# Kernel tuning notes

Hardware: AMD Instinct MI355X
Metric: run time of the kernel (lower is better)

The kernel has to match this reference:

```python
import jax, jax.numpy as jnp
import numpy as np

B = 4096
ED = 128          # EMBEDDING_DIM
HD = 64           # HIDDEN_DIM
LH = 128          # LSTM_HIDDEN_DIM
IN_DIM = ED * (12 + 48 + 1)  # 7808
N_ABILITY, N_MOVE = 300, 900


def setup_inputs() -> dict:
    key = jax.random.key(0)
    ks = jax.random.split(key, 16)
    s = lambda k, shape, scale=0.05: (jax.random.normal(k, shape, dtype=jnp.float32) * scale)
    return {
        "ability_ids": jax.random.randint(ks[0], (B, 12), 0, N_ABILITY),
        "move_ids": jax.random.randint(ks[1], (B, 48), 0, N_MOVE),
        "numerical": s(ks[2], (B, 84), 1.0),
        "mask": (jax.random.uniform(ks[3], (B, 9)) > 0.3).astype(jnp.float32),
        "h0": jnp.zeros((B, LH), jnp.float32),
        "c0": jnp.zeros((B, LH), jnp.float32),
        "ability_emb": s(ks[4], (N_ABILITY, ED), 1.0),
        "move_emb": s(ks[5], (N_MOVE, ED), 1.0),
        "num_W": s(ks[6], (ED, 84)),
        "num_b": s(ks[7], (ED,)),
        "Wih": s(ks[8], (4 * LH, IN_DIM), 0.01),
        "Whh": s(ks[9], (4 * LH, LH)),
        "bih": s(ks[10], (4 * LH,)),
        "bhh": s(ks[11], (4 * LH,)),
        "W1": s(ks[12], (HD, LH)),
        "b1": s(ks[13], (HD,)),
        "W2": s(ks[14], (ED, HD)),
        "b2": s(ks[15], (ED,)),
        "Wa": s(jax.random.fold_in(key, 100), (9, ED)),
        "ba": s(jax.random.fold_in(key, 101), (9,)),
    }


def reference(ability_ids, move_ids, numerical, mask, h0, c0,
              ability_emb, move_emb, num_W, num_b,
              Wih, Whh, bih, bhh, W1, b1, W2, b2, Wa, ba):
    # Gather + concat: [B, 12*ED] + [B, 48*ED] + [B, ED] -> [B, 7808]
    ab = ability_emb[ability_ids].reshape(ability_ids.shape[0], 12 * ED)
    mv = move_emb[move_ids].reshape(move_ids.shape[0], 48 * ED)
    num = numerical @ num_W.T + num_b
    x = jnp.concatenate([ab, mv, num], axis=-1)

    # Single-timestep LSTM (torch gate order: i, f, g, o)
    gates = x @ Wih.T + bih + h0 @ Whh.T + bhh
    i, f, g, o = jnp.split(gates, 4, axis=-1)
    i, f, o = jax.nn.sigmoid(i), jax.nn.sigmoid(f), jax.nn.sigmoid(o)
    g = jnp.tanh(g)
    c1 = f * c0 + i * g
    h1 = o * jnp.tanh(c1)

    # MLP head + action logits
    feat = jax.nn.relu(h1 @ W1.T + b1) @ W2.T + b2
    probs = jax.nn.softmax(feat @ Wa.T + ba, axis=-1)

    # Masked renormalization; fall back to unmasked probs when mask kills everything
    masked = probs * mask
    ssum = masked.sum(-1, keepdims=True)
    out = jnp.where(ssum > 0, masked / jnp.where(ssum > 0, ssum, 1.0), probs)
    return out, h1, c1
```

## Files before the change

### kernel.cpp

```cpp
#include <hip/hip_runtime.h>
#include <hip/hip_bf16.h>
#include <stdint.h>
#include <stddef.h>

typedef __bf16 bf16;
typedef __bf16 bf16x4 __attribute__((ext_vector_type(4)));
typedef __bf16 bf16x8 __attribute__((ext_vector_type(8)));
typedef float f32x4 __attribute__((ext_vector_type(4)));

#define BATCH 4096
#define KIH 7808
#define KTOT 7936
#define NG 512
#define LH 128
#define HD 64
#define ED 128
#define SPLITK 4

#define OFF_WCAT 0u
#define OFF_GPART 8126464u
#define OFF_XT   24903680u
#define OFF_AB   27000832u
#define OFF_MV   27077632u
#define OFF_ADDR 27308032u
#define OFF_H1B  28356608u
#define OFF_W1F  29405184u
#define OFF_W2F  29421568u
#define OFF_WAF  29437952u
#define OFF_NB   29442048u

#define O_H1 (BATCH * 9)
#define O_C1 (BATCH * 9 + BATCH * LH)

#define PREP_BP 2048
#define PREP_CW (PREP_BP + 512)
#define PREP_CE (PREP_CW + 150)
#define PREP_TOT (PREP_CE + 1)

typedef const __attribute__((address_space(1))) uint32_t* gas_ptr;
typedef __attribute__((address_space(3))) uint32_t* las_ptr;

__device__ __forceinline__ void async16(const void* g, void* l) {
    __builtin_amdgcn_global_load_lds((gas_ptr)g, (las_ptr)l, 16, 0, 0);
}

__global__ void prep(const int* __restrict__ ab_ids,
                     const int* __restrict__ mv_ids,
                     const float* __restrict__ numerical,
                     const float* __restrict__ h0,
                     const float* __restrict__ numW,
                     const float* __restrict__ numb,
                     const float* __restrict__ Wih,
                     const float* __restrict__ Whh,
                     const float* __restrict__ ab_emb,
                     const float* __restrict__ mv_emb,
                     const float* __restrict__ W1,
                     const float* __restrict__ W2,
                     const float* __restrict__ Wa,
                     uint8_t* __restrict__ ws) {
    const int bid = blockIdx.x;
    const int t = threadIdx.x;

    if (bid < PREP_BP) {
        bf16* xtail = (bf16*)(ws + OFF_XT);
        uint32_t* addrs = (uint32_t*)(ws + OFF_ADDR);
        const int h = t >> 7;
        const int th = t & 127;
        const int b = bid * 2 + h;

        __shared__ int ids[2][60];
        if (th < 60)
            ids[h][th] = (th < 12) ? ab_ids[b * 12 + th]
                                   : mv_ids[b * 48 + (th - 12)];

        const float v = (th < 84) ? numerical[(size_t)b * 84 + th] : 0.f;
        xtail[(size_t)b * 256 + th] = (bf16)v;
        xtail[(size_t)b * 256 + 128 + th] = (bf16)h0[(size_t)b * LH + th];
        __syncthreads();

        if (th < 64) {
            uint32_t off;
            if (th < 12) off = OFF_AB + (uint32_t)ids[h][th] * 256u;
            else if (th < 60) off = OFF_MV + (uint32_t)ids[h][th] * 256u;
            else if (th == 60) off = OFF_XT + (uint32_t)b * 512u;
            else if (th == 61) off = OFF_XT + (uint32_t)b * 512u + 256u;
            else off = OFF_XT;
            addrs[(size_t)b * 64 + th] = off;
        }
    } else if (bid < PREP_CW) {
        bf16* Wcat = (bf16*)(ws + OFF_WCAT);
        float* nbias = (float*)(ws + OFF_NB);
        const int n = bid - PREP_BP;

        __shared__ float wrow[128];
        __shared__ float nbs[128];
        if (t < 128) wrow[t] = Wih[(size_t)n * KIH + 7680 + t];
        else nbs[t - 128] = numb[t - 128];
        __syncthreads();

        const float* src_ih = Wih + (size_t)n * KIH;
        bf16* dst = Wcat + (size_t)n * KTOT;
        for (int k4 = t; k4 < 1920; k4 += 256) {
            const int k = k4 * 4;
            const float4 v = *(const float4*)(src_ih + k);
            bf16x4 o = {(bf16)v.x, (bf16)v.y, (bf16)v.z, (bf16)v.w};
            *(bf16x4*)(dst + k) = o;
        }
        if (t < 84) {
            float acc = 0.f;
#pragma unroll 4
            for (int e = 0; e < 128; ++e)
                acc += wrow[e] * numW[e * 84 + t];
            dst[7680 + t] = (bf16)acc;
        } else if (t < 128) {
            dst[7680 + t] = (bf16)0.f;
        } else {
            const int tt = t - 128;
            dst[KIH + tt] = (bf16)Whh[(size_t)n * LH + tt];
        }
        if (t == 255) {
            float a = 0.f;
#pragma unroll 4
            for (int e = 0; e < 128; ++e) a += wrow[e] * nbs[e];
            nbias[n] = a;
        }
    } else if (bid < PREP_CE) {
        bf16* ab8 = (bf16*)(ws + OFF_AB);
        bf16* mv8 = (bf16*)(ws + OFF_MV);
        const int i = ((bid - PREP_CW) * 256 + t) * 4;
        const bool isab = i < 300 * 128;
        const float4 v = isab ? *(const float4*)(ab_emb + i)
                              : *(const float4*)(mv_emb + (i - 300 * 128));
        bf16x4 o = {(bf16)v.x, (bf16)v.y, (bf16)v.z, (bf16)v.w};
        if (isab) *(bf16x4*)(ab8 + i) = o;
        else *(bf16x4*)(mv8 + (i - 300 * 128)) = o;
    } else {
        bf16* W1f = (bf16*)(ws + OFF_W1F);
        bf16* W2f = (bf16*)(ws + OFF_W2F);
        bf16* Waf = (bf16*)(ws + OFF_WAF);
        for (int e = t; e < 8192; e += 256) {
            const int j = e & 7, ln = (e >> 3) & 63, fid = e >> 9;
            const int kt = fid & 3, nt = fid >> 2;
            const int n = nt * 16 + (ln & 15);
            const int k = kt * 32 + (ln >> 4) * 8 + j;
            W1f[e] = (bf16)W1[n * 128 + k];
        }
        for (int e = t; e < 8192; e += 256) {
            const int j = e & 7, ln = (e >> 3) & 63, fid = e >> 9;
            const int kt = fid & 1, nt = fid >> 1;
            const int n = nt * 16 + (ln & 15);
            const int k = kt * 32 + (ln >> 4) * 8 + j;
            W2f[e] = (bf16)W2[n * 64 + k];
        }
        for (int e = t; e < 2048; e += 256) {
            const int j = e & 7, ln = (e >> 3) & 63, kt = e >> 9;
            const int n = ln & 15;
            const int k = kt * 32 + (ln >> 4) * 8 + j;
            Waf[e] = (n < 9) ? (bf16)Wa[n * 128 + k] : (bf16)0.f;
        }
    }
}

__global__ __launch_bounds__(256, 2) void gemm_gates(
    const uint8_t* __restrict__ wsbase,
    const bf16* __restrict__ Wcat,
    const uint32_t* __restrict__ addrs,
    bf16* __restrict__ gpart) {
    __shared__ bf16 As[2][128 * 64];
    __shared__ bf16 Bs[2][128 * 64];
    __shared__ uint32_t adr[17][128];

    const int tid = threadIdx.x;
    const int w = tid >> 6;
    const int lane = tid & 63;
    const int bm = blockIdx.x;
    const int bn = blockIdx.y;
    const int bz = blockIdx.z;
    const int kt_beg = bz * 31;
    const int kt_end = kt_beg + 31;

    const int s0 = kt_beg >> 1;
    const int ns = ((kt_end - 1) >> 1) - s0 + 1;
    for (int i = tid; i < ns * 128; i += 256) {
        adr[i >> 7][i & 127] =
            addrs[(size_t)(bm * 128 + (i & 127)) * 64 + s0 + (i >> 7)];
    }

    const int r_l = lane >> 3;
    const int sc16 = ((lane & 7) ^ r_l) * 16;

    const int wn = w & 1;
    const int wk = w >> 1;
    const int n0 = wn * 64;
    const int kk8 = wk * 4 + (lane >> 4);
    const int fl = lane & 15;

    f32x4 acc[8][4];
#pragma unroll
    for (int i = 0; i < 8; ++i)
#pragma unroll
        for (int j = 0; j < 4; ++j)
#pragma unroll
            for (int r = 0; r < 4; ++r) acc[i][j][r] = 0.f;

    __syncthreads();

    auto stage = [&](int kt, int pb) {
        const int k0 = kt * 64;
        const int sl = (kt >> 1) - s0;
        const int hb = (kt & 1) * 128;
#pragma unroll
        for (int j = 0; j < 4; ++j) {
            const int row = (w * 4 + j) * 8 + r_l;
            const uint8_t* gsrc = wsbase + adr[sl][row] + hb + sc16;
            async16(gsrc, (void*)&As[pb][((w * 4 + j) * 64 + lane) * 8]);
        }
#pragma unroll
        for (int j = 0; j < 4; ++j) {
            const int row = (w * 4 + j) * 8 + r_l;
            const bf16* gsrc = Wcat + (size_t)(bn * 128 + row) * KTOT + k0 + (sc16 >> 1);
            async16(gsrc, (void*)&Bs[pb][((w * 4 + j) * 64 + lane) * 8]);
        }
    };

    stage(kt_beg, 0);

    for (int kt = kt_beg; kt < kt_end; ++kt) {
        const int pb = (kt - kt_beg) & 1;
        __syncthreads();
        if (kt + 1 < kt_end) stage(kt + 1, pb ^ 1);

        const bf16* Ab = &As[pb][0];
        const bf16* Bb = &Bs[pb][0];

        bf16x8 bfr[4];
#pragma unroll
        for (int tj = 0; tj < 4; ++tj) {
            const int n = n0 + tj * 16 + fl;
            bfr[tj] = *(const bf16x8*)&Bb[n * 64 + ((kk8 ^ (n & 7)) * 8)];
        }
#pragma unroll
        for (int ti = 0; ti < 8; ++ti) {
            const int m = ti * 16 + fl;
            const bf16x8 af = *(const bf16x8*)&Ab[m * 64 + ((kk8 ^ (m & 7)) * 8)];
#pragma unroll
            for (int tj = 0; tj < 4; ++tj)
                acc[ti][tj] = __builtin_amdgcn_mfma_f32_16x16x32_bf16(
                    af, bfr[tj], acc[ti][tj], 0, 0, 0);
        }
    }

    __syncthreads();
    float* red = (wn == 0) ? (float*)&As[0][0] : (float*)&Bs[0][0];
    if (wk == 1) {
#pragma unroll
        for (int ti = 0; ti < 8; ++ti)
#pragma unroll
            for (int tj = 0; tj < 4; ++tj)
#pragma unroll
                for (int r = 0; r < 4; ++r)
                    red[((ti * 4 + tj) * 4 + r) * 64 + lane] = acc[ti][tj][r];
    }
    __syncthreads();

    if (wk == 0) {
        bf16* gdst = gpart + (size_t)bz * BATCH * NG;
        const int mlo = (lane >> 4) * 4;
#pragma unroll
        for (int ti = 0; ti < 8; ++ti)
#pragma unroll
            for (int tj = 0; tj < 4; ++tj) {
                const int mg = bm * 128 + ti * 16 + mlo;
                const int ng = bn * 128 + n0 + tj * 16 + fl;
                bf16* dst = gdst + (size_t)mg * NG + ng;
#pragma unroll
                for (int r = 0; r < 4; ++r)
                    dst[(size_t)r * NG] = (bf16)(
                        acc[ti][tj][r] + red[((ti * 4 + tj) * 4 + r) * 64 + lane]);
            }
    }
}

__global__ void reduce_lstm(const bf16* __restrict__ gpart,
                            const float* __restrict__ bih,
                            const float* __restrict__ bhh,
                            const float* __restrict__ nbias,
                            const float* __restrict__ c0,
                            float* __restrict__ out,
                            bf16* __restrict__ h1b) {
    const int t = threadIdx.x;
    const int b = blockIdx.x * 2 + (t >> 7);
    const int u = t & 127;

    float gv[4];
#pragma unroll
    for (int q = 0; q < 4; ++q)
        gv[q] = bih[q * 128 + u] + bhh[q * 128 + u] + nbias[q * 128 + u];
#pragma unroll
    for (int z = 0; z < SPLITK; ++z) {
        const bf16* gz = gpart + ((size_t)z * BATCH + b) * NG + u;
#pragma unroll
        for (int q = 0; q < 4; ++q) gv[q] += (float)gz[q * 128];
    }

    const float iv = 1.f / (1.f + __expf(-gv[0]));
    const float fv = 1.f / (1.f + __expf(-gv[1]));
    const float gg = tanhf(gv[2]);
    const float ov = 1.f / (1.f + __expf(-gv[3]));
    const float c1 = fv * c0[(size_t)b * LH + u] + iv * gg;
    const float h1 = ov * tanhf(c1);

    out[O_H1 + (size_t)b * LH + u] = h1;
    out[O_C1 + (size_t)b * LH + u] = c1;
    h1b[(size_t)b * LH + u] = (bf16)h1;
}

__global__ __launch_bounds__(64) void mlp_head(
    const bf16* __restrict__ h1b, const float* __restrict__ mask,
    const bf16* __restrict__ W1f, const bf16* __restrict__ W2f,
    const bf16* __restrict__ Waf,
    const float* __restrict__ b1, const float* __restrict__ b2,
    const float* __restrict__ ba,
    float* __restrict__ out) {
    __shared__ bf16 uS[16 * 64];
    __shared__ bf16 fS[16 * 128];

    const int lane = threadIdx.x;
    const int b0 = blockIdx.x * 16;
    const int nl = lane & 15, kg = lane >> 4;

    bf16x8 ah[4];
#pragma unroll
    for (int kt = 0; kt < 4; ++kt)
        ah[kt] = *(const bf16x8*)&h1b[(size_t)(b0 + nl) * 128 + kt * 32 + kg * 8];

#pragma unroll
    for (int nt = 0; nt < 4; ++nt) {
        f32x4 a = {0.f, 0.f, 0.f, 0.f};
#pragma unroll
        for (int kt = 0; kt < 4; ++kt)
            a = __builtin_amdgcn_mfma_f32_16x16x32_bf16(
                ah[kt], *(const bf16x8*)&W1f[((nt * 4 + kt) * 64 + lane) * 8],
                a, 0, 0, 0);
        const int n = nt * 16 + nl;
        const float bb = b1[n];
#pragma unroll
        for (int r = 0; r < 4; ++r)
            uS[(kg * 4 + r) * 64 + n] = (bf16)fmaxf(a[r] + bb, 0.f);
    }
    __syncthreads();

    bf16x8 au[2];
#pragma unroll
    for (int kt = 0; kt < 2; ++kt)
        au[kt] = *(const bf16x8*)&uS[nl * 64 + kt * 32 + kg * 8];

#pragma unroll
    for (int nt = 0; nt < 8; ++nt) {
        f32x4 a = {0.f, 0.f, 0.f, 0.f};
#pragma unroll
        for (int kt = 0; kt < 2; ++kt)
            a = __builtin_amdgcn_mfma_f32_16x16x32_bf16(
                au[kt], *(const bf16x8*)&W2f[((nt * 2 + kt) * 64 + lane) * 8],
                a, 0, 0, 0);
        const int n = nt * 16 + nl;
        const float bb = b2[n];
#pragma unroll
        for (int r = 0; r < 4; ++r)
            fS[(kg * 4 + r) * 128 + n] = (bf16)(a[r] + bb);
    }
    __syncthreads();

    bf16x8 afr[4];
#pragma unroll
    for (int kt = 0; kt < 4; ++kt)
        afr[kt] = *(const bf16x8*)&fS[nl * 128 + kt * 32 + kg * 8];

    f32x4 lg4 = {0.f, 0.f, 0.f, 0.f};
#pragma unroll
    for (int kt = 0; kt < 4; ++kt)
        lg4 = __builtin_amdgcn_mfma_f32_16x16x32_bf16(
            afr[kt], *(const bf16x8*)&Waf[(kt * 64 + lane) * 8], lg4, 0, 0, 0);

    const float bav = (nl < 9) ? ba[nl] : 0.f;

#pragma unroll
    for (int r = 0; r < 4; ++r) {
        const int b = b0 + kg * 4 + r;
        float lg = (nl < 9) ? lg4[r] + bav : -1e30f;
        float mx = lg;
#pragma unroll
        for (int off = 1; off < 16; off <<= 1)
            mx = fmaxf(mx, __shfl_xor(mx, off, 64));
        const float e = (nl < 9) ? __expf(lg - mx) : 0.f;
        const float mv = (nl < 9) ? mask[(size_t)b * 9 + nl] : 0.f;
        float tot = e, ms = e * mv;
#pragma unroll
        for (int off = 1; off < 16; off <<= 1) {
            tot += __shfl_xor(tot, off, 64);
            ms += __shfl_xor(ms, off, 64);
        }
        if (nl < 9)
            out[(size_t)b * 9 + nl] = (ms > 0.f) ? e * mv / ms : e / tot;
    }
}

extern "C" void kernel_launch(void* const* d_in, const int* in_sizes, int n_in,
                              void* d_out, int out_size, void* d_ws, size_t ws_size,
                              hipStream_t stream) {
    const int* ab_ids = (const int*)d_in[0];
    const int* mv_ids = (const int*)d_in[1];
    const float* numerical = (const float*)d_in[2];
    const float* mask = (const float*)d_in[3];
    const float* h0 = (const float*)d_in[4];
    const float* c0 = (const float*)d_in[5];
    const float* ab_emb = (const float*)d_in[6];
    const float* mv_emb = (const float*)d_in[7];
    const float* numW = (const float*)d_in[8];
    const float* numb = (const float*)d_in[9];
    const float* Wih = (const float*)d_in[10];
    const float* Whh = (const float*)d_in[11];
    const float* bih = (const float*)d_in[12];
    const float* bhh = (const float*)d_in[13];
    const float* W1 = (const float*)d_in[14];
    const float* b1 = (const float*)d_in[15];
    const float* W2 = (const float*)d_in[16];
    const float* b2 = (const float*)d_in[17];
    const float* Wa = (const float*)d_in[18];
    const float* ba = (const float*)d_in[19];
    float* out = (float*)d_out;

    uint8_t* ws = (uint8_t*)d_ws;
    bf16* Wcat = (bf16*)(ws + OFF_WCAT);
    bf16* gpart = (bf16*)(ws + OFF_GPART);
    uint32_t* addrs = (uint32_t*)(ws + OFF_ADDR);
    bf16* h1b = (bf16*)(ws + OFF_H1B);
    bf16* W1f = (bf16*)(ws + OFF_W1F);
    bf16* W2f = (bf16*)(ws + OFF_W2F);
    bf16* Waf = (bf16*)(ws + OFF_WAF);
    float* nbias = (float*)(ws + OFF_NB);

    prep<<<PREP_TOT, 256, 0, stream>>>(
        ab_ids, mv_ids, numerical, h0, numW, numb, Wih, Whh, ab_emb, mv_emb,
        W1, W2, Wa, ws);
    gemm_gates<<<dim3(32, 4, SPLITK), 256, 0, stream>>>(ws, Wcat, addrs, gpart);
    reduce_lstm<<<BATCH / 2, 256, 0, stream>>>(gpart, bih, bhh, nbias, c0,
                                               out, h1b);
    mlp_head<<<BATCH / 16, 64, 0, stream>>>(h1b, mask, W1f, W2f, Waf,
                                            b1, b2, ba, out);
}
```

Baseline: 169.0 us.

## Fuse four kernels into one cooperative persistent kernel with grid syncs

Replaces the prep, split-K gate GEMM, LSTM reduce and MLP head launches with a single cooperative kernel of 512 blocks that uses grid.sync between phases. The LSTM reduction and MLP head are also merged, so h1 stays in shared memory instead of being written out and read back. The aim is to remove launch gaps and one global round-trip. The cost is that all blocks must be co-resident (launch bounds of 2 blocks per CU), plus grid-wide barrier overhead and idle blocks in the tail phase. It falls back to the old multi-kernel path if the cooperative launch fails.

Result: slower. 420.3 us (+148.7%).

```diff
diff --git a/kernel.cpp b/kernel.cpp
--- a/kernel.cpp
+++ b/kernel.cpp
@@ -1,4 +1,5 @@
 #include <hip/hip_runtime.h>
+#include <hip/hip_cooperative_groups.h>
 #include <hip/hip_bf16.h>
 #include <stdint.h>
 #include <stddef.h>
@@ -16,6 +17,7 @@
 #define HD 64
 #define ED 128
 #define SPLITK 4
+#define GRID 512
 
 #define OFF_WCAT 0u
 #define OFF_GPART 8126464u
@@ -402,6 +404,396 @@
         }
         if (nl < 9)
             out[(size_t)b * 9 + nl] = (ms > 0.f) ? e * mv / ms : e / tot;
+    }
+}
+
+__global__ __launch_bounds__(256, 2) void fused(
+    const int* __restrict__ ab_ids, const int* __restrict__ mv_ids,
+    const float* __restrict__ numerical, const float* __restrict__ mask,
+    const float* __restrict__ h0, const float* __restrict__ c0,
+    const float* __restrict__ ab_emb, const float* __restrict__ mv_emb,
+    const float* __restrict__ numW, const float* __restrict__ numb,
+    const float* __restrict__ Wih, const float* __restrict__ Whh,
+    const float* __restrict__ bih, const float* __restrict__ bhh,
+    const float* __restrict__ W1, const float* __restrict__ b1,
+    const float* __restrict__ W2, const float* __restrict__ b2,
+    const float* __restrict__ Wa, const float* __restrict__ ba,
+    uint8_t* __restrict__ ws, float* __restrict__ out) {
+
+    __shared__ bf16 As[2][128 * 64];
+    __shared__ bf16 Bs[2][128 * 64];
+    __shared__ uint32_t adr[17][128];
+
+    const int bid = blockIdx.x;
+    const int t = threadIdx.x;
+    cooperative_groups::grid_group grid = cooperative_groups::this_grid();
+
+    for (int vb = bid; vb < PREP_TOT; vb += GRID) {
+        if (vb < PREP_BP) {
+            bf16* xtail = (bf16*)(ws + OFF_XT);
+            uint32_t* addrs = (uint32_t*)(ws + OFF_ADDR);
+            int* ids = (int*)&adr[0][0];
+            const int h = t >> 7;
+            const int th = t & 127;
+            const int b = vb * 2 + h;
+
+            if (th < 60)
+                ids[h * 60 + th] = (th < 12) ? ab_ids[b * 12 + th]
+                                             : mv_ids[b * 48 + (th - 12)];
+
+            const float v = (th < 84) ? numerical[(size_t)b * 84 + th] : 0.f;
+            xtail[(size_t)b * 256 + th] = (bf16)v;
+            xtail[(size_t)b * 256 + 128 + th] = (bf16)h0[(size_t)b * LH + th];
+            __syncthreads();
+
+            if (th < 64) {
+                uint32_t off;
+                if (th < 12) off = OFF_AB + (uint32_t)ids[h * 60 + th] * 256u;
+                else if (th < 60) off = OFF_MV + (uint32_t)ids[h * 60 + th] * 256u;
+                else if (th == 60) off = OFF_XT + (uint32_t)b * 512u;
+                else if (th == 61) off = OFF_XT + (uint32_t)b * 512u + 256u;
+                else off = OFF_XT;
+                addrs[(size_t)b * 64 + th] = off;
+            }
+        } else if (vb < PREP_CW) {
+            bf16* Wcat = (bf16*)(ws + OFF_WCAT);
+            float* nbias = (float*)(ws + OFF_NB);
+            const int n = vb - PREP_BP;
+            float* wrow = (float*)&As[0][0];
+            float* nbs = wrow + 128;
+
+            if (t < 128) wrow[t] = Wih[(size_t)n * KIH + 7680 + t];
+            else if (t < 256) nbs[t - 128] = numb[t - 128];
+            __syncthreads();
+
+            const float* src_ih = Wih + (size_t)n * KIH;
+            bf16* dst = Wcat + (size_t)n * KTOT;
+            for (int k4 = t; k4 < 1920; k4 += 256) {
+                const int k = k4 * 4;
+                const float4 v = *(const float4*)(src_ih + k);
+                bf16x4 o = {(bf16)v.x, (bf16)v.y, (bf16)v.z, (bf16)v.w};
+                *(bf16x4*)(dst + k) = o;
+            }
+            if (t < 84) {
+                float acc = 0.f;
+#pragma unroll 4
+                for (int e = 0; e < 128; ++e)
+                    acc += wrow[e] * numW[e * 84 + t];
+                dst[7680 + t] = (bf16)acc;
+            } else if (t < 128) {
+                dst[7680 + t] = (bf16)0.f;
+            } else {
+                const int tt = t - 128;
+                dst[KIH + tt] = (bf16)Whh[(size_t)n * LH + tt];
+            }
+            if (t == 255) {
+                float a = 0.f;
+#pragma unroll 4
+                for (int e = 0; e < 128; ++e) a += wrow[e] * nbs[e];
+                nbias[n] = a;
+            }
+        } else if (vb < PREP_CE) {
+            bf16* ab8 = (bf16*)(ws + OFF_AB);
+            bf16* mv8 = (bf16*)(ws + OFF_MV);
+            const int i = ((vb - PREP_CW) * 256 + t) * 4;
+            const bool isab = i < 300 * 128;
+            const float4 v = isab ? *(const float4*)(ab_emb + i)
+                                  : *(const float4*)(mv_emb + (i - 300 * 128));
+            bf16x4 o = {(bf16)v.x, (bf16)v.y, (bf16)v.z, (bf16)v.w};
+            if (isab) *(bf16x4*)(ab8 + i) = o;
+            else *(bf16x4*)(mv8 + (i - 300 * 128)) = o;
+        } else {
+            bf16* W1f = (bf16*)(ws + OFF_W1F);
+            bf16* W2f = (bf16*)(ws + OFF_W2F);
+            bf16* Waf = (bf16*)(ws + OFF_WAF);
+            for (int e = t; e < 8192; e += 256) {
+                const int j = e & 7, ln = (e >> 3) & 63, fid = e >> 9;
+                const int kt = fid & 3, nt = fid >> 2;
+                const int n = nt * 16 + (ln & 15);
+                const int k = kt * 32 + (ln >> 4) * 8 + j;
+                W1f[e] = (bf16)W1[n * 128 + k];
+            }
+            for (int e = t; e < 8192; e += 256) {
+                const int j = e & 7, ln = (e >> 3) & 63, fid = e >> 9;
+                const int kt = fid & 1, nt = fid >> 1;
+                const int n = nt * 16 + (ln & 15);
+                const int k = kt * 32 + (ln >> 4) * 8 + j;
+                W2f[e] = (bf16)W2[n * 64 + k];
+            }
+            for (int e = t; e < 2048; e += 256) {
+                const int j = e & 7, ln = (e >> 3) & 63, kt = e >> 9;
+                const int n = ln & 15;
+                const int k = kt * 32 + (ln >> 4) * 8 + j;
+                Waf[e] = (n < 9) ? (bf16)Wa[n * 128 + k] : (bf16)0.f;
+            }
+        }
+        __syncthreads();
+    }
+
+    __threadfence();
+    grid.sync();
+
+    {
+        const uint8_t* wsbase = ws;
+        const bf16* Wcat = (const bf16*)(ws + OFF_WCAT);
+        const uint32_t* addrs = (const uint32_t*)(ws + OFF_ADDR);
+        bf16* gpart = (bf16*)(ws + OFF_GPART);
+
+        const int w = t >> 6;
+        const int lane = t & 63;
+        const int bm = bid & 31;
+        const int bn = (bid >> 5) & 3;
+        const int bz = bid >> 7;
+        const int kt_beg = bz * 31;
+        const int kt_end = kt_beg + 31;
+
+        const int s0 = kt_beg >> 1;
+        const int ns = ((kt_end - 1) >> 1) - s0 + 1;
+        for (int i = t; i < ns * 128; i += 256) {
+            adr[i >> 7][i & 127] =
+                addrs[(size_t)(bm * 128 + (i & 127)) * 64 + s0 + (i >> 7)];
+        }
+
+        const int r_l = lane >> 3;
+        const int sc16 = ((lane & 7) ^ r_l) * 16;
+
+        const int wn = w & 1;
+        const int wk = w >> 1;
+        const int n0 = wn * 64;
+        const int kk8 = wk * 4 + (lane >> 4);
+        const int fl = lane & 15;
+
+        f32x4 acc[8][4];
+#pragma unroll
+        for (int i = 0; i < 8; ++i)
+#pragma unroll
+            for (int j = 0; j < 4; ++j)
+#pragma unroll
+                for (int r = 0; r < 4; ++r) acc[i][j][r] = 0.f;
+
+        __syncthreads();
+
+        auto stage = [&](int kt, int pb) {
+            const int k0 = kt * 64;
+            const int sl = (kt >> 1) - s0;
+            const int hb = (kt & 1) * 128;
+#pragma unroll
+            for (int j = 0; j < 4; ++j) {
+                const int row = (w * 4 + j) * 8 + r_l;
+                const uint8_t* gsrc = wsbase + adr[sl][row] + hb + sc16;
+                async16(gsrc, (void*)&As[pb][((w * 4 + j) * 64 + lane) * 8]);
+            }
+#pragma unroll
+            for (int j = 0; j < 4; ++j) {
+                const int row = (w * 4 + j) * 8 + r_l;
+                const bf16* gsrc = Wcat + (size_t)(bn * 128 + row) * KTOT + k0 + (sc16 >> 1);
+                async16(gsrc, (void*)&Bs[pb][((w * 4 + j) * 64 + lane) * 8]);
+            }
+        };
+
+        stage(kt_beg, 0);
+
+        for (int kt = kt_beg; kt < kt_end; ++kt) {
+            const int pb = (kt - kt_beg) & 1;
+            __syncthreads();
+            if (kt + 1 < kt_end) stage(kt + 1, pb ^ 1);
+
+            const bf16* Ab = &As[pb][0];
+            const bf16* Bb = &Bs[pb][0];
+
+            bf16x8 bfr[4];
+#pragma unroll
+            for (int tj = 0; tj < 4; ++tj) {
+                const int n = n0 + tj * 16 + fl;
+                bfr[tj] = *(const bf16x8*)&Bb[n * 64 + ((kk8 ^ (n & 7)) * 8)];
+            }
+#pragma unroll
+            for (int ti = 0; ti < 8; ++ti) {
+                const int m = ti * 16 + fl;
+                const bf16x8 af = *(const bf16x8*)&Ab[m * 64 + ((kk8 ^ (m & 7)) * 8)];
+#pragma unroll
+                for (int tj = 0; tj < 4; ++tj)
+                    acc[ti][tj] = __builtin_amdgcn_mfma_f32_16x16x32_bf16(
+                        af, bfr[tj], acc[ti][tj], 0, 0, 0);
+            }
+        }
+
+        __syncthreads();
+        float* red = (wn == 0) ? (float*)&As[0][0] : (float*)&Bs[0][0];
+        if (wk == 1) {
+#pragma unroll
+            for (int ti = 0; ti < 8; ++ti)
+#pragma unroll
+                for (int tj = 0; tj < 4; ++tj)
+#pragma unroll
+                    for (int r = 0; r < 4; ++r)
+                        red[((ti * 4 + tj) * 4 + r) * 64 + lane] = acc[ti][tj][r];
+        }
+        __syncthreads();
+
+        if (wk == 0) {
+            bf16* gdst = gpart + (size_t)bz * BATCH * NG;
+            const int mlo = (lane >> 4) * 4;
+#pragma unroll
+            for (int ti = 0; ti < 8; ++ti)
+#pragma unroll
+                for (int tj = 0; tj < 4; ++tj) {
+                    const int mg = bm * 128 + ti * 16 + mlo;
+                    const int ng = bn * 128 + n0 + tj * 16 + fl;
+                    bf16* dst = gdst + (size_t)mg * NG + ng;
+#pragma unroll
+                    for (int r = 0; r < 4; ++r)
+                        dst[(size_t)r * NG] = (bf16)(
+                            acc[ti][tj][r] + red[((ti * 4 + tj) * 4 + r) * 64 + lane]);
+                }
+        }
+    }
+
+    __threadfence();
+    grid.sync();
+
+    if (bid < 256) {
+        const bf16* gpart = (const bf16*)(ws + OFF_GPART);
+        const float* nbias = (const float*)(ws + OFF_NB);
+        bf16* hS = (bf16*)&As[0][0];
+        bf16* uS = (bf16*)&Bs[0][0];
+        bf16* fS = uS + 16 * 64;
+
+        {
+            const int r = t >> 4;
+            const int uc = (t & 15) * 8;
+            const int b = bid * 16 + r;
+
+            float gv[4][8];
+#pragma unroll
+            for (int q = 0; q < 4; ++q)
+#pragma unroll
+                for (int hh = 0; hh < 2; ++hh) {
+                    const f32x4 va = *(const f32x4*)(bih + q * 128 + uc + hh * 4);
+                    const f32x4 vb = *(const f32x4*)(bhh + q * 128 + uc + hh * 4);
+                    const f32x4 vn = *(const f32x4*)(nbias + q * 128 + uc + hh * 4);
+#pragma unroll
+                    for (int j = 0; j < 4; ++j)
+                        gv[q][hh * 4 + j] = va[j] + vb[j] + vn[j];
+                }
+#pragma unroll
+            for (int z = 0; z < SPLITK; ++z) {
+                const bf16* gz = gpart + ((size_t)z * BATCH + b) * NG;
+#pragma unroll
+                for (int q = 0; q < 4; ++q) {
+                    const bf16x8 v = *(const bf16x8*)(gz + q * 128 + uc);
+#pragma unroll
+                    for (int j = 0; j < 8; ++j) gv[q][j] += (float)v[j];
+                }
+            }
+
+            const f32x4 c0a = *(const f32x4*)(c0 + (size_t)b * LH + uc);
+            const f32x4 c0b = *(const f32x4*)(c0 + (size_t)b * LH + uc + 4);
+            float h1v[8], c1v[8];
+#pragma unroll
+            for (int j = 0; j < 8; ++j) {
+                const float iv = 1.f / (1.f + __expf(-gv[0][j]));
+                const float fv = 1.f / (1.f + __expf(-gv[1][j]));
+                const float gg = tanhf(gv[2][j]);
+                const float ov = 1.f / (1.f + __expf(-gv[3][j]));
+                const float c0j = (j < 4) ? c0a[j] : c0b[j - 4];
+                const float c1 = fv * c0j + iv * gg;
+                const float h1 = ov * tanhf(c1);
+                c1v[j] = c1;
+                h1v[j] = h1;
+                hS[r * 128 + uc + j] = (bf16)h1;
+            }
+            *(f32x4*)(out + O_H1 + (size_t)b * LH + uc) = *(const f32x4*)&h1v[0];
+            *(f32x4*)(out + O_H1 + (size_t)b * LH + uc + 4) = *(const f32x4*)&h1v[4];
+            *(f32x4*)(out + O_C1 + (size_t)b * LH + uc) = *(const f32x4*)&c1v[0];
+            *(f32x4*)(out + O_C1 + (size_t)b * LH + uc + 4) = *(const f32x4*)&c1v[4];
+        }
+        __syncthreads();
+
+        const bf16* W1f = (const bf16*)(ws + OFF_W1F);
+        const bf16* W2f = (const bf16*)(ws + OFF_W2F);
+        const bf16* Waf = (const bf16*)(ws + OFF_WAF);
+        const int nl = t & 15, kg = (t & 63) >> 4;
+        const int b0 = bid * 16;
+
+        if (t < 64) {
+            bf16x8 ah[4];
+#pragma unroll
+            for (int kt = 0; kt < 4; ++kt)
+                ah[kt] = *(const bf16x8*)&hS[nl * 128 + kt * 32 + kg * 8];
+#pragma unroll
+            for (int nt = 0; nt < 4; ++nt) {
+                f32x4 a = {0.f, 0.f, 0.f, 0.f};
+#pragma unroll
+                for (int kt = 0; kt < 4; ++kt)
+                    a = __builtin_amdgcn_mfma_f32_16x16x32_bf16(
+                        ah[kt], *(const bf16x8*)&W1f[((nt * 4 + kt) * 64 + t) * 8],
+                        a, 0, 0, 0);
+                const int n = nt * 16 + nl;
+                const float bb = b1[n];
+#pragma unroll
+                for (int rr = 0; rr < 4; ++rr)
+                    uS[(kg * 4 + rr) * 64 + n] = (bf16)fmaxf(a[rr] + bb, 0.f);
+            }
+        }
+        __syncthreads();
+
+        if (t < 64) {
+            bf16x8 au[2];
+#pragma unroll
+            for (int kt = 0; kt < 2; ++kt)
+                au[kt] = *(const bf16x8*)&uS[nl * 64 + kt * 32 + kg * 8];
+#pragma unroll
+            for (int nt = 0; nt < 8; ++nt) {
+                f32x4 a = {0.f, 0.f, 0.f, 0.f};
+#pragma unroll
+                for (int kt = 0; kt < 2; ++kt)
+                    a = __builtin_amdgcn_mfma_f32_16x16x32_bf16(
+                        au[kt], *(const bf16x8*)&W2f[((nt * 2 + kt) * 64 + t) * 8],
+                        a, 0, 0, 0);
+                const int n = nt * 16 + nl;
+                const float bb = b2[n];
+#pragma unroll
+                for (int rr = 0; rr < 4; ++rr)
+                    fS[(kg * 4 + rr) * 128 + n] = (bf16)(a[rr] + bb);
+            }
+        }
+        __syncthreads();
+
+        if (t < 64) {
+            bf16x8 afr[4];
+#pragma unroll
+            for (int kt = 0; kt < 4; ++kt)
+                afr[kt] = *(const bf16x8*)&fS[nl * 128 + kt * 32 + kg * 8];
+
+            f32x4 lg4 = {0.f, 0.f, 0.f, 0.f};
+#pragma unroll
+            for (int kt = 0; kt < 4; ++kt)
+                lg4 = __builtin_amdgcn_mfma_f32_16x16x32_bf16(
+                    afr[kt], *(const bf16x8*)&Waf[(kt * 64 + t) * 8], lg4, 0, 0, 0);
+
+            const float bav = (nl < 9) ? ba[nl] : 0.f;
+
+#pragma unroll
+            for (int rr = 0; rr < 4; ++rr) {
+                const int b = b0 + kg * 4 + rr;
+                float lg = (nl < 9) ? lg4[rr] + bav : -1e30f;
+                float mx = lg;
+#pragma unroll
+                for (int off = 1; off < 16; off <<= 1)
+                    mx = fmaxf(mx, __shfl_xor(mx, off, 64));
+                const float e = (nl < 9) ? __expf(lg - mx) : 0.f;
+                const float mv = (nl < 9) ? mask[(size_t)b * 9 + nl] : 0.f;
+                float tot = e, ms = e * mv;
+#pragma unroll
+                for (int off = 1; off < 16; off <<= 1) {
+                    tot += __shfl_xor(tot, off, 64);
+                    ms += __shfl_xor(ms, off, 64);
+                }
+                if (nl < 9)
+                    out[(size_t)b * 9 + nl] = (ms > 0.f) ? e * mv / ms : e / tot;
+            }
+        }
     }
 }
 
@@ -429,23 +821,48 @@
     const float* Wa = (const float*)d_in[18];
     const float* ba = (const float*)d_in[19];
     float* out = (float*)d_out;
-
     uint8_t* ws = (uint8_t*)d_ws;
-    bf16* Wcat = (bf16*)(ws + OFF_WCAT);
-    bf16* gpart = (bf16*)(ws + OFF_GPART);
-    uint32_t* addrs = (uint32_t*)(ws + OFF_ADDR);
-    bf16* h1b = (bf16*)(ws + OFF_H1B);
-    bf16* W1f = (bf16*)(ws + OFF_W1F);
-    bf16* W2f = (bf16*)(ws + OFF_W2F);
-    bf16* Waf = (bf16*)(ws + OFF_WAF);
-    float* nbias = (float*)(ws + OFF_NB);
-
-    prep<<<PREP_TOT, 256, 0, stream>>>(
-        ab_ids, mv_ids, numerical, h0, numW, numb, Wih, Whh, ab_emb, mv_emb,
-        W1, W2, Wa, ws);
-    gemm_gates<<<dim3(32, 4, SPLITK), 256, 0, stream>>>(ws, Wcat, addrs, gpart);
-    reduce_lstm<<<BATCH / 2, 256, 0, stream>>>(gpart, bih, bhh, nbias, c0,
-                                               out, h1b);
-    mlp_head<<<BATCH / 16, 64, 0, stream>>>(h1b, mask, W1f, W2f, Waf,
-                                            b1, b2, ba, out);
+
+    static int s_coop = -1;
+    if (s_coop < 0) {
+        int dev = 0;
+        hipGetDevice(&dev);
+        int v = 0;
+        hipDeviceGetAttribute(&v, hipDeviceAttributeCooperativeLaunch, dev);
+        s_coop = v;
+    }
+
+    bool launched = false;
+    if (s_coop) {
+        void* args[22] = {
+            (void*)&ab_ids, (void*)&mv_ids, (void*)&numerical, (void*)&mask,
+            (void*)&h0, (void*)&c0, (void*)&ab_emb, (void*)&mv_emb,
+            (void*)&numW, (void*)&numb, (void*)&Wih, (void*)&Whh,
+            (void*)&bih, (void*)&bhh, (void*)&W1, (void*)&b1,
+            (void*)&W2, (void*)&b2, (void*)&Wa, (void*)&ba,
+            (void*)&ws, (void*)&out};
+        launched = (hipLaunchCooperativeKernel((const void*)fused, dim3(GRID),
+                                               dim3(256), args, 0, stream) ==
+                    hipSuccess);
+    }
+
+    if (!launched) {
+        bf16* Wcat = (bf16*)(ws + OFF_WCAT);
+        bf16* gpart = (bf16*)(ws + OFF_GPART);
+        uint32_t* addrs = (uint32_t*)(ws + OFF_ADDR);
+        bf16* h1b = (bf16*)(ws + OFF_H1B);
+        bf16* W1f = (bf16*)(ws + OFF_W1F);
+        bf16* W2f = (bf16*)(ws + OFF_W2F);
+        bf16* Waf = (bf16*)(ws + OFF_WAF);
+        float* nbias = (float*)(ws + OFF_NB);
+
+        prep<<<PREP_TOT, 256, 0, stream>>>(
+            ab_ids, mv_ids, numerical, h0, numW, numb, Wih, Whh, ab_emb, mv_emb,
+            W1, W2, Wa, ws);
+        gemm_gates<<<dim3(32, 4, SPLITK), 256, 0, stream>>>(ws, Wcat, addrs, gpart);
+        reduce_lstm<<<BATCH / 2, 256, 0, stream>>>(gpart, bih, bhh, nbias, c0,
+                                                   out, h1b);
+        mlp_head<<<BATCH / 16, 64, 0, stream>>>(h1b, mask, W1f, W2f, Waf,
+                                                b1, b2, ba, out);
+    }
 }
```

## Fuse LSTM reduction with MLP head and remap GEMM blocks per XCD

Applied to the files above, without the earlier changes.

The split-K reduction plus LSTM cell and the MLP/softmax head are merged into one tail kernel. h1 now stays in shared memory as bf16 instead of going through a global workspace buffer, which removes one launch and a global round-trip. The reduction loads are vectorised, each thread handling 8 units. Separately, the GEMM grid is flattened to 1D and block ids are remapped so that blocks landing on the same XCD share a bn column, for better L2 reuse of weight tiles. The cost is that only one of the four waves in each tail block does the MLP work, leaving the rest idle during that phase.

Result: no change. 168.4 us (-0.3%).

```diff
diff --git a/kernel.cpp b/kernel.cpp
--- a/kernel.cpp
+++ b/kernel.cpp
@@ -23,7 +23,6 @@
 #define OFF_AB   27000832u
 #define OFF_MV   27077632u
 #define OFF_ADDR 27308032u
-#define OFF_H1B  28356608u
 #define OFF_W1F  29405184u
 #define OFF_W2F  29421568u
 #define OFF_WAF  29437952u
@@ -173,9 +172,15 @@
     const int tid = threadIdx.x;
     const int w = tid >> 6;
     const int lane = tid & 63;
-    const int bm = blockIdx.x;
-    const int bn = blockIdx.y;
-    const int bz = blockIdx.z;
+
+    const int bid = blockIdx.x;
+    const int xcd = bid & 7;
+    const int slot = bid >> 3;
+    const int bn = xcd & 3;
+    const int combo = ((xcd >> 2) << 6) + slot;
+    const int bm = combo & 31;
+    const int bz = combo >> 5;
+
     const int kt_beg = bz * 31;
     const int kt_end = kt_beg + 31;
 
@@ -281,127 +286,156 @@
     }
 }
 
-__global__ void reduce_lstm(const bf16* __restrict__ gpart,
-                            const float* __restrict__ bih,
-                            const float* __restrict__ bhh,
-                            const float* __restrict__ nbias,
-                            const float* __restrict__ c0,
-                            float* __restrict__ out,
-                            bf16* __restrict__ h1b) {
-    const int t = threadIdx.x;
-    const int b = blockIdx.x * 2 + (t >> 7);
-    const int u = t & 127;
-
-    float gv[4];
-#pragma unroll
-    for (int q = 0; q < 4; ++q)
-        gv[q] = bih[q * 128 + u] + bhh[q * 128 + u] + nbias[q * 128 + u];
-#pragma unroll
-    for (int z = 0; z < SPLITK; ++z) {
-        const bf16* gz = gpart + ((size_t)z * BATCH + b) * NG + u;
-#pragma unroll
-        for (int q = 0; q < 4; ++q) gv[q] += (float)gz[q * 128];
-    }
-
-    const float iv = 1.f / (1.f + __expf(-gv[0]));
-    const float fv = 1.f / (1.f + __expf(-gv[1]));
-    const float gg = tanhf(gv[2]);
-    const float ov = 1.f / (1.f + __expf(-gv[3]));
-    const float c1 = fv * c0[(size_t)b * LH + u] + iv * gg;
-    const float h1 = ov * tanhf(c1);
-
-    out[O_H1 + (size_t)b * LH + u] = h1;
-    out[O_C1 + (size_t)b * LH + u] = c1;
-    h1b[(size_t)b * LH + u] = (bf16)h1;
-}
-
-__global__ __launch_bounds__(64) void mlp_head(
-    const bf16* __restrict__ h1b, const float* __restrict__ mask,
+__global__ __launch_bounds__(256) void tail(
+    const bf16* __restrict__ gpart,
+    const float* __restrict__ bih, const float* __restrict__ bhh,
+    const float* __restrict__ nbias, const float* __restrict__ c0,
+    const float* __restrict__ mask,
     const bf16* __restrict__ W1f, const bf16* __restrict__ W2f,
     const bf16* __restrict__ Waf,
     const float* __restrict__ b1, const float* __restrict__ b2,
     const float* __restrict__ ba,
     float* __restrict__ out) {
+    __shared__ bf16 hS[16 * 128];
     __shared__ bf16 uS[16 * 64];
     __shared__ bf16 fS[16 * 128];
 
-    const int lane = threadIdx.x;
-    const int b0 = blockIdx.x * 16;
-    const int nl = lane & 15, kg = lane >> 4;
-
-    bf16x8 ah[4];
-#pragma unroll
-    for (int kt = 0; kt < 4; ++kt)
-        ah[kt] = *(const bf16x8*)&h1b[(size_t)(b0 + nl) * 128 + kt * 32 + kg * 8];
-
-#pragma unroll
-    for (int nt = 0; nt < 4; ++nt) {
-        f32x4 a = {0.f, 0.f, 0.f, 0.f};
+    const int t = threadIdx.x;
+    const int bid = blockIdx.x;
+    const int b0 = bid * 16;
+
+    {
+        const int r = t >> 4;
+        const int uc = (t & 15) * 8;
+        const int b = b0 + r;
+
+        float gv[4][8];
+#pragma unroll
+        for (int q = 0; q < 4; ++q)
+#pragma unroll
+            for (int hh = 0; hh < 2; ++hh) {
+                const f32x4 va = *(const f32x4*)(bih + q * 128 + uc + hh * 4);
+                const f32x4 vb = *(const f32x4*)(bhh + q * 128 + uc + hh * 4);
+                const f32x4 vn = *(const f32x4*)(nbias + q * 128 + uc + hh * 4);
+#pragma unroll
+                for (int j = 0; j < 4; ++j)
+                    gv[q][hh * 4 + j] = va[j] + vb[j] + vn[j];
+            }
+#pragma unroll
+        for (int z = 0; z < SPLITK; ++z) {
+            const bf16* gz = gpart + ((size_t)z * BATCH + b) * NG;
+#pragma unroll
+            for (int q = 0; q < 4; ++q) {
+                const bf16x8 v = *(const bf16x8*)(gz + q * 128 + uc);
+#pragma unroll
+                for (int j = 0; j < 8; ++j) gv[q][j] += (float)v[j];
+            }
+        }
+
+        const f32x4 c0a = *(const f32x4*)(c0 + (size_t)b * LH + uc);
+        const f32x4 c0b = *(const f32x4*)(c0 + (size_t)b * LH + uc + 4);
+        float h1v[8], c1v[8];
+        bf16x8 hv8;
+#pragma unroll
+        for (int j = 0; j < 8; ++j) {
+            const float iv = 1.f / (1.f + __expf(-gv[0][j]));
+            const float fv = 1.f / (1.f + __expf(-gv[1][j]));
+            const float gg = tanhf(gv[2][j]);
+            const float ov = 1.f / (1.f + __expf(-gv[3][j]));
+            const float c0j = (j < 4) ? c0a[j] : c0b[j - 4];
+            const float c1 = fv * c0j + iv * gg;
+            const float h1 = ov * tanhf(c1);
+            c1v[j] = c1;
+            h1v[j] = h1;
+            hv8[j] = (bf16)h1;
+        }
+        *(bf16x8*)&hS[r * 128 + uc] = hv8;
+        *(f32x4*)(out + O_H1 + (size_t)b * LH + uc) = *(const f32x4*)&h1v[0];
+        *(f32x4*)(out + O_H1 + (size_t)b * LH + uc + 4) = *(const f32x4*)&h1v[4];
+        *(f32x4*)(out + O_C1 + (size_t)b * LH + uc) = *(const f32x4*)&c1v[0];
+        *(f32x4*)(out + O_C1 + (size_t)b * LH + uc + 4) = *(const f32x4*)&c1v[4];
+    }
+    __syncthreads();
+
+    const int nl = t & 15, kg = (t & 63) >> 4;
+
+    if (t < 64) {
+        bf16x8 ah[4];
 #pragma unroll
         for (int kt = 0; kt < 4; ++kt)
-            a = __builtin_amdgcn_mfma_f32_16x16x32_bf16(
-                ah[kt], *(const bf16x8*)&W1f[((nt * 4 + kt) * 64 + lane) * 8],
-                a, 0, 0, 0);
-        const int n = nt * 16 + nl;
-        const float bb = b1[n];
-#pragma unroll
-        for (int r = 0; r < 4; ++r)
-            uS[(kg * 4 + r) * 64 + n] = (bf16)fmaxf(a[r] + bb, 0.f);
-    }
-    __syncthreads();
-
-    bf16x8 au[2];
-#pragma unroll
-    for (int kt = 0; kt < 2; ++kt)
-        au[kt] = *(const bf16x8*)&uS[nl * 64 + kt * 32 + kg * 8];
-
-#pragma unroll
-    for (int nt = 0; nt < 8; ++nt) {
-        f32x4 a = {0.f, 0.f, 0.f, 0.f};
+            ah[kt] = *(const bf16x8*)&hS[nl * 128 + kt * 32 + kg * 8];
+#pragma unroll
+        for (int nt = 0; nt < 4; ++nt) {
+            f32x4 a = {0.f, 0.f, 0.f, 0.f};
+#pragma unroll
+            for (int kt = 0; kt < 4; ++kt)
+                a = __builtin_amdgcn_mfma_f32_16x16x32_bf16(
+                    ah[kt], *(const bf16x8*)&W1f[((nt * 4 + kt) * 64 + t) * 8],
+                    a, 0, 0, 0);
+            const int n = nt * 16 + nl;
+            const float bb = b1[n];
+#pragma unroll
+            for (int rr = 0; rr < 4; ++rr)
+                uS[(kg * 4 + rr) * 64 + n] = (bf16)fmaxf(a[rr] + bb, 0.f);
+        }
+    }
+    __syncthreads();
+
+    if (t < 64) {
+        bf16x8 au[2];
 #pragma unroll
         for (int kt = 0; kt < 2; ++kt)
-            a = __builtin_amdgcn_mfma_f32_16x16x32_bf16(
-                au[kt], *(const bf16x8*)&W2f[((nt * 2 + kt) * 64 + lane) * 8],
-                a, 0, 0, 0);
-        const int n = nt * 16 + nl;
-        const float bb = b2[n];
-#pragma unroll
-        for (int r = 0; r < 4; ++r)
-            fS[(kg * 4 + r) * 128 + n] = (bf16)(a[r] + bb);
-    }
-    __syncthreads();
-
-    bf16x8 afr[4];
-#pragma unroll
-    for (int kt = 0; kt < 4; ++kt)
-        afr[kt] = *(const bf16x8*)&fS[nl * 128 + kt * 32 + kg * 8];
-
-    f32x4 lg4 = {0.f, 0.f, 0.f, 0.f};
-#pragma unroll
-    for (int kt = 0; kt < 4; ++kt)
-        lg4 = __builtin_amdgcn_mfma_f32_16x16x32_bf16(
-            afr[kt], *(const bf16x8*)&Waf[(kt * 64 + lane) * 8], lg4, 0, 0, 0);
-
-    const float bav = (nl < 9) ? ba[nl] : 0.f;
-
-#pragma unroll
-    for (int r = 0; r < 4; ++r) {
-        const int b = b0 + kg * 4 + r;
-        float lg = (nl < 9) ? lg4[r] + bav : -1e30f;
-        float mx = lg;
-#pragma unroll
-        for (int off = 1; off < 16; off <<= 1)
-            mx = fmaxf(mx, __shfl_xor(mx, off, 64));
-        const float e = (nl < 9) ? __expf(lg - mx) : 0.f;
-        const float mv = (nl < 9) ? mask[(size_t)b * 9 + nl] : 0.f;
-        float tot = e, ms = e * mv;
-#pragma unroll
-        for (int off = 1; off < 16; off <<= 1) {
-            tot += __shfl_xor(tot, off, 64);
-            ms += __shfl_xor(ms, off, 64);
-        }
-        if (nl < 9)
-            out[(size_t)b * 9 + nl] = (ms > 0.f) ? e * mv / ms : e / tot;
+            au[kt] = *(const bf16x8*)&uS[nl * 64 + kt * 32 + kg * 8];
+#pragma unroll
+        for (int nt = 0; nt < 8; ++nt) {
+            f32x4 a = {0.f, 0.f, 0.f, 0.f};
+#pragma unroll
+            for (int kt = 0; kt < 2; ++kt)
+                a = __builtin_amdgcn_mfma_f32_16x16x32_bf16(
+                    au[kt], *(const bf16x8*)&W2f[((nt * 2 + kt) * 64 + t) * 8],
+                    a, 0, 0, 0);
+            const int n = nt * 16 + nl;
+            const float bb = b2[n];
+#pragma unroll
+            for (int rr = 0; rr < 4; ++rr)
+                fS[(kg * 4 + rr) * 128 + n] = (bf16)(a[rr] + bb);
+        }
+    }
+    __syncthreads();
+
+    if (t < 64) {
+        bf16x8 afr[4];
+#pragma unroll
+        for (int kt = 0; kt < 4; ++kt)
+            afr[kt] = *(const bf16x8*)&fS[nl * 128 + kt * 32 + kg * 8];
+
+        f32x4 lg4 = {0.f, 0.f, 0.f, 0.f};
+#pragma unroll
+        for (int kt = 0; kt < 4; ++kt)
+            lg4 = __builtin_amdgcn_mfma_f32_16x16x32_bf16(
+                afr[kt], *(const bf16x8*)&Waf[(kt * 64 + t) * 8], lg4, 0, 0, 0);
+
+        const float bav = (nl < 9) ? ba[nl] : 0.f;
+
+#pragma unroll
+        for (int rr = 0; rr < 4; ++rr) {
+            const int b = b0 + kg * 4 + rr;
+            float lg = (nl < 9) ? lg4[rr] + bav : -1e30f;
+            float mx = lg;
+#pragma unroll
+            for (int off = 1; off < 16; off <<= 1)
+                mx = fmaxf(mx, __shfl_xor(mx, off, 64));
+            const float e = (nl < 9) ? __expf(lg - mx) : 0.f;
+            const float mv = (nl < 9) ? mask[(size_t)b * 9 + nl] : 0.f;
+            float tot = e, ms = e * mv;
+#pragma unroll
+            for (int off = 1; off < 16; off <<= 1) {
+                tot += __shfl_xor(tot, off, 64);
+                ms += __shfl_xor(ms, off, 64);
+            }
+            if (nl < 9)
+                out[(size_t)b * 9 + nl] = (ms > 0.f) ? e * mv / ms : e / tot;
+        }
     }
 }
 
@@ -434,7 +468,6 @@
     bf16* Wcat = (bf16*)(ws + OFF_WCAT);
     bf16* gpart = (bf16*)(ws + OFF_GPART);
     uint32_t* addrs = (uint32_t*)(ws + OFF_ADDR);
-    bf16* h1b = (bf16*)(ws + OFF_H1B);
     bf16* W1f = (bf16*)(ws + OFF_W1F);
     bf16* W2f = (bf16*)(ws + OFF_W2F);
     bf16* Waf = (bf16*)(ws + OFF_WAF);
@@ -443,9 +476,7 @@
     prep<<<PREP_TOT, 256, 0, stream>>>(
         ab_ids, mv_ids, numerical, h0, numW, numb, Wih, Whh, ab_emb, mv_emb,
         W1, W2, Wa, ws);
-    gemm_gates<<<dim3(32, 4, SPLITK), 256, 0, stream>>>(ws, Wcat, addrs, gpart);
-    reduce_lstm<<<BATCH / 2, 256, 0, stream>>>(gpart, bih, bhh, nbias, c0,
-                                               out, h1b);
-    mlp_head<<<BATCH / 16, 64, 0, stream>>>(h1b, mask, W1f, W2f, Waf,
-                                            b1, b2, ba, out);
+    gemm_gates<<<512, 256, 0, stream>>>(ws, Wcat, addrs, gpart);
+    tail<<<BATCH / 16, 256, 0, stream>>>(gpart, bih, bhh, nbias, c0, mask,
+                                         W1f, W2f, Waf, b1, b2, ba, out);
 }
```
